# Performance work log

Hardware: AMD Instinct MI355X
Metric: run time of the kernel (lower is better)

## Reference

```python
import jax, jax.numpy as jnp
import numpy as np

# V:N:M sparsity config (n=2 kept of m=8 per vector-block; mask pattern [1,0,1,0,0,0,0,0])
M_BLK = 8
KEEP_OFFSETS = np.array([0, 2], dtype=np.int32)  # positions kept in each m-block
B, S, D_IN, D_OUT = 2, 8192, 4096, 4096
K_KEPT = D_IN // M_BLK * len(KEEP_OFFSETS)  # 1024


def _keep_idx():
    # column indices of the surviving weight entries (same for every output row)
    blocks = np.arange(D_IN // M_BLK, dtype=np.int32)[:, None] * M_BLK  # [D_IN/M,1]
    return jnp.asarray((blocks + KEEP_OFFSETS[None, :]).reshape(-1))   # [K_KEPT]


def setup_inputs() -> dict:
    key = jax.random.key(0)
    k1, k2, k3 = jax.random.split(key, 3)
    x = jax.random.normal(k1, (B, S, D_IN), dtype=jnp.float32)
    values = jax.random.normal(k2, (D_OUT, K_KEPT), dtype=jnp.float32) * 0.02
    bias = jax.random.normal(k3, (D_OUT,), dtype=jnp.float32) * 0.02
    return {"x": x, "values": values, "bias": bias}


def reference(x, values, bias):
    # Sparse SpMM: gather kept input features, dense GEMM with compressed values.
    # Equivalent to x @ (masked dense W).T + bias, without materializing W.
    keep = _keep_idx()               # [K_KEPT] int32, constant metadata
    xg = x[..., keep]                # [B,S,K_KEPT]
    out = jnp.einsum('bsk,nk->bsn', xg, values) + bias  # [B,S,D_OUT]
    return out
```

## Files before the change

kernel.cpp:

```cpp
#include <hip/hip_runtime.h>
#include <hip/hip_bf16.h>


#define M_TOTAL 16384
#define DIN     4096
#define KDIM    1024
#define NDIM    4096

typedef unsigned short u16;
typedef unsigned int   u32;
typedef __bf16 bf16x8 __attribute__((ext_vector_type(8)));
typedef float  f32x4  __attribute__((ext_vector_type(4)));

typedef const void __attribute__((address_space(1)))* gp_t;
typedef void __attribute__((address_space(3)))*       lp_t;

__device__ __forceinline__ u16 f2bf(float f) {
    u32 u = __float_as_uint(f);
    u += 0x7FFFu + ((u >> 16) & 1u);
    return (u16)(u >> 16);
}
__device__ __forceinline__ u32 pack2(float a, float b) {
    return (u32)f2bf(a) | ((u32)f2bf(b) << 16);
}

__global__ void prep_kernel(const float* __restrict__ x, uint2* __restrict__ xg2,
                            const float* __restrict__ vals, uint4* __restrict__ vb4) {
    const int tid = threadIdx.x;
    if (blockIdx.x < 4096) {
        int i = blockIdx.x * 256 + tid;
        const int stride = 4096 * 256;
#pragma unroll
        for (int it = 0; it < 4; ++it, i += stride) {
            const f32x4* p = (const f32x4*)(x + (size_t)i * 16);
            f32x4 f0 = __builtin_nontemporal_load(p);
            f32x4 f1 = __builtin_nontemporal_load(p + 2);
            xg2[i] = make_uint2(pack2(f0.x, f0.z), pack2(f1.x, f1.z));
        }
    } else {
        const int i = (blockIdx.x - 4096) * 256 + tid;
        const f32x4* p = (const f32x4*)(vals + (size_t)i * 8);
        f32x4 a = __builtin_nontemporal_load(p);
        f32x4 b = __builtin_nontemporal_load(p + 1);
        vb4[i] = make_uint4(pack2(a.x, a.y), pack2(a.z, a.w),
                            pack2(b.x, b.y), pack2(b.z, b.w));
    }
}


#define LDSA(d, kh) (((d) * 2 + (kh)) * 16384)
#define LDSB(d, kh) (65536 + ((d) * 2 + (kh)) * 16384)

#define LOADA(d, kh, mh) { _Pragma("unroll") \
    for (int m_ = 0; m_ < 4; ++m_) \
        af[m_] = *(const bf16x8*)(lds + LDSA(d, kh) + (wr * 8 + (mh) * 4 + m_) * 1024 + fl_off); }

#define LOADB(d, kh) { _Pragma("unroll") \
    for (int n_ = 0; n_ < 4; ++n_) \
        bfr[n_] = *(const bf16x8*)(lds + LDSB(d, kh) + (wc * 4 + n_) * 1024 + fl_off); }

#define MFMA16(mh) { \
    __builtin_amdgcn_s_setprio(1); \
    _Pragma("unroll") for (int m_ = 0; m_ < 4; ++m_) \
    _Pragma("unroll") for (int n_ = 0; n_ < 4; ++n_) \
        acc[(mh) * 4 + m_][n_] = __builtin_amdgcn_mfma_f32_16x16x32_bf16( \
            af[m_], bfr[n_], acc[(mh) * 4 + m_][n_], 0, 0, 0); \
    __builtin_amdgcn_s_setprio(0); }

#define BAR() __builtin_amdgcn_s_barrier()
#define VMCNT6() asm volatile("s_waitcnt vmcnt(6)" ::: "memory")

__global__ __launch_bounds__(512, 2) void gemm_kernel(
    const u16* __restrict__ A, const u16* __restrict__ Bv,
    const float* __restrict__ bias, float* __restrict__ C)
{
    __shared__ __align__(1024) char lds[131072];

    const int tid  = threadIdx.x;
    const int lane = tid & 63;
    const int wid  = tid >> 6;
    const int wr   = wid >> 2;
    const int wc   = wid & 3;
    const int lrow = lane & 15;
    const int lg   = lane >> 4;

    const int bb   = blockIdx.x;
    const int btm0 = (bb & 7) * 8 + (bb >> 7);
    const int btn  = (bb >> 3) & 15;

    const int st_r0 = wid * 16 + (lane >> 2);
    const int st_ck = ((lane & 3) * 8) ^ ((lane & 32) >> 1);
    const u16* A0  = A  + (size_t)(btm0 * 256 + st_r0) * KDIM + st_ck;
    const u16* Bs0 = Bv + (size_t)(btn  * 256 + st_r0) * KDIM + st_ck;
    const int dst0 = tid * 16;

    const int fl_off = lrow * 64 + ((lg * 16) ^ (((lrow >> 3) & 1) << 5));

    auto STAGE = [&](const u16* as_, int s) {
        const int kt = s >> 2, j = s & 3;
        const int d = kt & 1, kh = (j >> 1) & 1;
        const int ko = kt * 64 + kh * 32;
        const u16* src = (j & 1) ? Bs0 : as_;
        const int base = ((j & 1) ? 65536 : 0) + (d * 2 + kh) * 16384;
        __builtin_amdgcn_global_load_lds((gp_t)(src + ko),
            (lp_t)(lds + base + dst0), 16, 0, 0);
        __builtin_amdgcn_global_load_lds((gp_t)(src + 128 * KDIM + ko),
            (lp_t)(lds + base + 8192 + dst0), 16, 0, 0);
    };

    const int c_col0 = btn * 256 + wc * 64 + lrow;
    float bvr[4];
#pragma unroll
    for (int n = 0; n < 4; ++n) bvr[n] = bias[c_col0 + n * 16];

    f32x4 acc[8][4] = {};
    bf16x8 af[4], bfr[4];

    STAGE(A0, 0); STAGE(A0, 1); STAGE(A0, 2); STAGE(A0, 3);
    STAGE(A0, 4); STAGE(A0, 5); STAGE(A0, 6);
    VMCNT6();
    BAR();

#pragma unroll 1
    for (int r = 0; r < 4; ++r) {
        const u16* Ar = A0 + (size_t)r * 512 * KDIM;
        const u16* An = (r < 3) ? (Ar + 512 * KDIM) : Ar;

#pragma unroll 1
        for (int t = 0; t < 7; ++t) {
            const int s0 = 8 * t + 7;
            LOADB(0, 0); LOADA(0, 0, 0); STAGE(Ar, s0);     BAR(); MFMA16(0); BAR();
            LOADA(0, 0, 1);              STAGE(Ar, s0 + 1); BAR(); MFMA16(1); BAR();
            LOADB(0, 1); LOADA(0, 1, 0); STAGE(Ar, s0 + 2); BAR(); MFMA16(0); BAR();
            LOADA(0, 1, 1);              STAGE(Ar, s0 + 3); BAR(); MFMA16(1);
            VMCNT6(); BAR();
            LOADB(1, 0); LOADA(1, 0, 0); STAGE(Ar, s0 + 4); BAR(); MFMA16(0); BAR();
            LOADA(1, 0, 1);              STAGE(Ar, s0 + 5); BAR(); MFMA16(1); BAR();
            LOADB(1, 1); LOADA(1, 1, 0); STAGE(Ar, s0 + 6); BAR(); MFMA16(0); BAR();
            LOADA(1, 1, 1);              STAGE(Ar, s0 + 7); BAR(); MFMA16(1);
            VMCNT6(); BAR();
        }
        LOADB(0, 0); LOADA(0, 0, 0); STAGE(Ar, 63); BAR(); MFMA16(0); BAR();
        LOADA(0, 0, 1);              STAGE(An, 0);  BAR(); MFMA16(1); BAR();
        LOADB(0, 1); LOADA(0, 1, 0); STAGE(An, 1);  BAR(); MFMA16(0); BAR();
        LOADA(0, 1, 1);              STAGE(An, 2);  BAR(); MFMA16(1);
        VMCNT6(); BAR();
        LOADB(1, 0); LOADA(1, 0, 0); STAGE(An, 3);  BAR(); MFMA16(0); BAR();
        LOADA(1, 0, 1);              STAGE(An, 4);  BAR(); MFMA16(1); BAR();
        LOADB(1, 1); LOADA(1, 1, 0); STAGE(An, 5);  BAR(); MFMA16(0); BAR();
        LOADA(1, 1, 1);              STAGE(An, 6);  BAR(); MFMA16(1);
        VMCNT6(); BAR();

        const int c_row0 = (btm0 + 2 * r) * 256 + wr * 128 + lg * 4;
#pragma unroll
        for (int mi = 0; mi < 8; ++mi) {
            const int row = c_row0 + (mi >> 2) * 64 + (mi & 3) * 16;
#pragma unroll
            for (int n = 0; n < 4; ++n) {
#pragma unroll
                for (int j = 0; j < 4; ++j)
                    __builtin_nontemporal_store(acc[mi][n][j] + bvr[n],
                        &C[(size_t)(row + j) * NDIM + c_col0 + n * 16]);
                acc[mi][n] = (f32x4){0.f, 0.f, 0.f, 0.f};
            }
        }
    }
}

extern "C" void kernel_launch(void* const* d_in, const int* in_sizes, int n_in,
                              void* d_out, int out_size, void* d_ws, size_t ws_size,
                              hipStream_t stream) {
    const float* x      = (const float*)d_in[0];
    const float* values = (const float*)d_in[1];
    const float* bias   = (const float*)d_in[2];
    float* out = (float*)d_out;

    u16* xg = (u16*)d_ws;
    u16* vb = (u16*)((char*)d_ws + ((size_t)32 << 20));

    prep_kernel<<<6144, 256, 0, stream>>>(x, (uint2*)xg, values, (uint4*)vb);
    gemm_kernel<<<256, 512, 0, stream>>>(xg, vb, bias, out);
}
```

Before: 212.4 us.

## Switch GEMM inner loop from 16x16x32 to 32x32x16 bf16 MFMA tiles

Replaces the 16x16x32 MFMA micro-tiles with 32x32x16 MFMA instructions, each consuming two K-slices per accumulator. The LDS fragment addressing and the swizzle in both the global-to-LDS staging and the fragment reads are reworked to match the 32-row operand layout. The epilogue is rewritten for the 32x32 accumulator register layout. The goal is fewer MFMA issues and fewer operand reads per FLOP, at the cost of a more complex swizzle whose correctness and LDS bank behaviour must hold.

Result: faster. 205.7 us (median of 3 runs) (-3.2%).

```diff
diff --git a/kernel.cpp b/kernel.cpp
--- a/kernel.cpp
+++ b/kernel.cpp
@@ -11,6 +11,7 @@
 typedef unsigned int   u32;
 typedef __bf16 bf16x8 __attribute__((ext_vector_type(8)));
 typedef float  f32x4  __attribute__((ext_vector_type(4)));
+typedef float  f32x16 __attribute__((ext_vector_type(16)));
 
 typedef const void __attribute__((address_space(1)))* gp_t;
 typedef void __attribute__((address_space(3)))*       lp_t;
@@ -52,19 +53,26 @@
 #define LDSB(d, kh) (65536 + ((d) * 2 + (kh)) * 16384)
 
 #define LOADA(d, kh, mh) { _Pragma("unroll") \
-    for (int m_ = 0; m_ < 4; ++m_) \
-        af[m_] = *(const bf16x8*)(lds + LDSA(d, kh) + (wr * 8 + (mh) * 4 + m_) * 1024 + fl_off); }
+    for (int mm = 0; mm < 2; ++mm) { _Pragma("unroll") \
+    for (int ks = 0; ks < 2; ++ks) \
+        af[mm * 2 + ks] = *(const bf16x8*)(lds + LDSA(d, kh) \
+            + (wr * 8 + ((mh) * 2 + mm) * 2) * 1024 + fl_base \
+            + (((ks << 5) + acol) ^ aswz)); } }
 
 #define LOADB(d, kh) { _Pragma("unroll") \
-    for (int n_ = 0; n_ < 4; ++n_) \
-        bfr[n_] = *(const bf16x8*)(lds + LDSB(d, kh) + (wc * 4 + n_) * 1024 + fl_off); }
+    for (int nn = 0; nn < 2; ++nn) { _Pragma("unroll") \
+    for (int ks = 0; ks < 2; ++ks) \
+        bfr[nn * 2 + ks] = *(const bf16x8*)(lds + LDSB(d, kh) \
+            + (wc * 4 + nn * 2) * 1024 + fl_base \
+            + (((ks << 5) + acol) ^ aswz)); } }
 
-#define MFMA16(mh) { \
+#define MFMA8(mh) { \
     __builtin_amdgcn_s_setprio(1); \
-    _Pragma("unroll") for (int m_ = 0; m_ < 4; ++m_) \
-    _Pragma("unroll") for (int n_ = 0; n_ < 4; ++n_) \
-        acc[(mh) * 4 + m_][n_] = __builtin_amdgcn_mfma_f32_16x16x32_bf16( \
-            af[m_], bfr[n_], acc[(mh) * 4 + m_][n_], 0, 0, 0); \
+    _Pragma("unroll") for (int mm = 0; mm < 2; ++mm) \
+    _Pragma("unroll") for (int nn = 0; nn < 2; ++nn) \
+    _Pragma("unroll") for (int ks = 0; ks < 2; ++ks) \
+        acc[(mh) * 2 + mm][nn] = __builtin_amdgcn_mfma_f32_32x32x16_bf16( \
+            af[mm * 2 + ks], bfr[nn * 2 + ks], acc[(mh) * 2 + mm][nn], 0, 0, 0); \
     __builtin_amdgcn_s_setprio(0); }
 
 #define BAR() __builtin_amdgcn_s_barrier()
@@ -81,20 +89,20 @@
     const int wid  = tid >> 6;
     const int wr   = wid >> 2;
     const int wc   = wid & 3;
-    const int lrow = lane & 15;
-    const int lg   = lane >> 4;
 
     const int bb   = blockIdx.x;
     const int btm0 = (bb & 7) * 8 + (bb >> 7);
     const int btn  = (bb >> 3) & 15;
 
     const int st_r0 = wid * 16 + (lane >> 2);
-    const int st_ck = ((lane & 3) * 8) ^ ((lane & 32) >> 1);
+    const int st_ck = ((lane & 3) * 8) ^ ((tid & 32) >> 1) ^ ((tid & 64) >> 3);
     const u16* A0  = A  + (size_t)(btm0 * 256 + st_r0) * KDIM + st_ck;
     const u16* Bs0 = Bv + (size_t)(btn  * 256 + st_r0) * KDIM + st_ck;
     const int dst0 = tid * 16;
 
-    const int fl_off = lrow * 64 + ((lg * 16) ^ (((lrow >> 3) & 1) << 5));
+    const int fl_base = (lane & 15) * 64 + ((lane >> 4) & 1) * 1024;
+    const int aswz    = (((lane >> 3) & 1) << 5) ^ (((lane >> 4) & 1) << 4);
+    const int acol    = ((lane >> 5) & 1) * 16;
 
     auto STAGE = [&](const u16* as_, int s) {
         const int kt = s >> 2, j = s & 3;
@@ -108,12 +116,12 @@
             (lp_t)(lds + base + 8192 + dst0), 16, 0, 0);
     };
 
-    const int c_col0 = btn * 256 + wc * 64 + lrow;
-    float bvr[4];
+    const int c_colb = btn * 256 + wc * 64 + (lane & 31);
+    float bvr[2];
 #pragma unroll
-    for (int n = 0; n < 4; ++n) bvr[n] = bias[c_col0 + n * 16];
+    for (int n = 0; n < 2; ++n) bvr[n] = bias[c_colb + n * 32];
 
-    f32x4 acc[8][4] = {};
+    f32x16 acc[4][2] = {};
     bf16x8 af[4], bfr[4];
 
     STAGE(A0, 0); STAGE(A0, 1); STAGE(A0, 2); STAGE(A0, 3);
@@ -129,39 +137,45 @@
 #pragma unroll 1
         for (int t = 0; t < 7; ++t) {
             const int s0 = 8 * t + 7;
-            LOADB(0, 0); LOADA(0, 0, 0); STAGE(Ar, s0);     BAR(); MFMA16(0); BAR();
-            LOADA(0, 0, 1);              STAGE(Ar, s0 + 1); BAR(); MFMA16(1); BAR();
-            LOADB(0, 1); LOADA(0, 1, 0); STAGE(Ar, s0 + 2); BAR(); MFMA16(0); BAR();
-            LOADA(0, 1, 1);              STAGE(Ar, s0 + 3); BAR(); MFMA16(1);
+            LOADB(0, 0); LOADA(0, 0, 0); STAGE(Ar, s0);     BAR(); MFMA8(0); BAR();
+            LOADA(0, 0, 1);              STAGE(Ar, s0 + 1); BAR(); MFMA8(1); BAR();
+            LOADB(0, 1); LOADA(0, 1, 0); STAGE(Ar, s0 + 2); BAR(); MFMA8(0); BAR();
+            LOADA(0, 1, 1);              STAGE(Ar, s0 + 3); BAR(); MFMA8(1);
             VMCNT6(); BAR();
-            LOADB(1, 0); LOADA(1, 0, 0); STAGE(Ar, s0 + 4); BAR(); MFMA16(0); BAR();
-            LOADA(1, 0, 1);              STAGE(Ar, s0 + 5); BAR(); MFMA16(1); BAR();
-            LOADB(1, 1); LOADA(1, 1, 0); STAGE(Ar, s0 + 6); BAR(); MFMA16(0); BAR();
-            LOADA(1, 1, 1);              STAGE(Ar, s0 + 7); BAR(); MFMA16(1);
+            LOADB(1, 0); LOADA(1, 0, 0); STAGE(Ar, s0 + 4); BAR(); MFMA8(0); BAR();
+            LOADA(1, 0, 1);              STAGE(Ar, s0 + 5); BAR(); MFMA8(1); BAR();
+            LOADB(1, 1); LOADA(1, 1, 0); STAGE(Ar, s0 + 6); BAR(); MFMA8(0); BAR();
+            LOADA(1, 1, 1);              STAGE(Ar, s0 + 7); BAR(); MFMA8(1);
             VMCNT6(); BAR();
         }
-        LOADB(0, 0); LOADA(0, 0, 0); STAGE(Ar, 63); BAR(); MFMA16(0); BAR();
-        LOADA(0, 0, 1);              STAGE(An, 0);  BAR(); MFMA16(1); BAR();
-        LOADB(0, 1); LOADA(0, 1, 0); STAGE(An, 1);  BAR(); MFMA16(0); BAR();
-        LOADA(0, 1, 1);              STAGE(An, 2);  BAR(); MFMA16(1);
+        LOADB(0, 0); LOADA(0, 0, 0); STAGE(Ar, 63); BAR(); MFMA8(0); BAR();
+        LOADA(0, 0, 1);              STAGE(An, 0);  BAR(); MFMA8(1); BAR();
+        LOADB(0, 1); LOADA(0, 1, 0); STAGE(An, 1);  BAR(); MFMA8(0); BAR();
+        LOADA(0, 1, 1);              STAGE(An, 2);  BAR(); MFMA8(1);
         VMCNT6(); BAR();
-        LOADB(1, 0); LOADA(1, 0, 0); STAGE(An, 3);  BAR(); MFMA16(0); BAR();
-        LOADA(1, 0, 1);              STAGE(An, 4);  BAR(); MFMA16(1); BAR();
-        LOADB(1, 1); LOADA(1, 1, 0); STAGE(An, 5);  BAR(); MFMA16(0); BAR();
-        LOADA(1, 1, 1);              STAGE(An, 6);  BAR(); MFMA16(1);
+        LOADB(1, 0); LOADA(1, 0, 0); STAGE(An, 3);  BAR(); MFMA8(0); BAR();
+        LOADA(1, 0, 1);              STAGE(An, 4);  BAR(); MFMA8(1); BAR();
+        LOADB(1, 1); LOADA(1, 1, 0); STAGE(An, 5);  BAR(); MFMA8(0); BAR();
+        LOADA(1, 1, 1);              STAGE(An, 6);  BAR(); MFMA8(1);
         VMCNT6(); BAR();
 
-        const int c_row0 = (btm0 + 2 * r) * 256 + wr * 128 + lg * 4;
+        const int c_row0 = (btm0 + 2 * r) * 256 + wr * 128 + ((lane >> 5) & 1) * 4;
 #pragma unroll
-        for (int mi = 0; mi < 8; ++mi) {
-            const int row = c_row0 + (mi >> 2) * 64 + (mi & 3) * 16;
+        for (int mi = 0; mi < 4; ++mi) {
 #pragma unroll
-            for (int n = 0; n < 4; ++n) {
+            for (int n = 0; n < 2; ++n) {
+                f32x16 a = acc[mi][n];
 #pragma unroll
-                for (int j = 0; j < 4; ++j)
-                    __builtin_nontemporal_store(acc[mi][n][j] + bvr[n],
-                        &C[(size_t)(row + j) * NDIM + c_col0 + n * 16]);
-                acc[mi][n] = (f32x4){0.f, 0.f, 0.f, 0.f};
+                for (int q = 0; q < 4; ++q) {
+#pragma unroll
+                    for (int rr = 0; rr < 4; ++rr) {
+                        const int row = c_row0 + mi * 32 + q * 8 + rr;
+                        __builtin_nontemporal_store(a[q * 4 + rr] + bvr[n],
+                            &C[(size_t)row * NDIM + c_colb + n * 32]);
+                    }
+                }
+#pragma unroll
+                for (int z = 0; z < 16; ++z) acc[mi][n][z] = 0.f;
             }
         }
     }
```
